# Kernel tuning notes

Hardware: AMD Instinct MI355X
Metric: run time of the kernel (lower is better)

Reference implementation:

```python
import jax, jax.numpy as jnp
import numpy as np

LOWER_T = 6.0
UPPER_T = 50.0


def _conv(x, w, pad_h, pad_w):
    # x: [N,1,H,W] or [N,Cin,H,W]; w: [O,I,kh,kw]; cross-correlation like torch Conv2d
    return jax.lax.conv_general_dilated(
        x, w, window_strides=(1, 1),
        padding=[(pad_h, pad_h), (pad_w, pad_w)],
        dimension_numbers=('NCHW', 'OIHW', 'NCHW'))


def setup_inputs() -> dict:
    key = jax.random.key(0)
    H = W = 4096
    img = jax.random.uniform(key, (1, 3, H, W), dtype=jnp.float32) * 255.0

    # scipy.signal.gaussian(5, std=1.0), unnormalized window
    std = 1.0
    g = np.exp(-0.5 * ((np.arange(5, dtype=np.float32) - 2.0) / std) ** 2).astype(np.float32)
    gauss = jnp.asarray(g)  # [5]

    sobel = jnp.asarray(np.array([[1, 0, -1], [2, 0, -2], [1, 0, -1]], dtype=np.float32))  # [3,3]

    f = np.zeros((8, 1, 3, 3), dtype=np.float32)
    f[:, 0, 1, 1] = 1.0
    offs = [(1, 2), (2, 2), (2, 1), (2, 0), (1, 0), (0, 0), (0, 1), (0, 2)]  # 0,45,...,315 deg
    for k, (r, c) in enumerate(offs):
        f[k, 0, r, c] = -1.0
    dir_w = jnp.asarray(f)  # [8,1,3,3]

    return {"img": img, "gauss": gauss, "sobel": sobel, "dir_w": dir_w}


def reference(img, gauss, sobel, dir_w):
    N, C, H, W = img.shape  # N == 1, C == 3
    x = img.reshape(C, 1, H, W)  # treat channels as batch

    # separable gaussian blur: 1x5 then 5x1, padding 2 (matches torch Conv2d)
    gw_h = gauss.reshape(1, 1, 1, 5)
    gw_v = gauss.reshape(1, 1, 5, 1)
    blurred = _conv(_conv(x, gw_h, 0, 2), gw_v, 2, 0)  # [3,1,H,W]

    sw_h = sobel.reshape(1, 1, 3, 3)
    sw_v = sobel.T.reshape(1, 1, 3, 3)
    gx = _conv(blurred, sw_h, 1, 1)  # [3,1,H,W]
    gy = _conv(blurred, sw_v, 1, 1)

    # per-channel magnitude summed over RGB -> [1,1,H,W]
    grad_mag = jnp.sqrt(gx * gx + gy * gy + 1e-8).sum(axis=0, keepdims=True)[:, 0:1]

    gx_sum = gx.sum(axis=0, keepdims=True)[:, 0:1]
    gy_sum = gy.sum(axis=0, keepdims=True)[:, 0:1]
    ori = jnp.arctan2(gy_sum, gx_sum) * (180.0 / 3.14159) + 180.0
    ori = jnp.round(ori / 45.0) * 45.0

    all_filtered = _conv(grad_mag, dir_w, 1, 1)  # [1,8,H,W]

    idx_pos = jnp.mod(ori / 45.0, 8.0).astype(jnp.int32)          # [1,1,H,W]
    idx_neg = jnp.mod(ori / 45.0 + 4.0, 8.0).astype(jnp.int32)

    cs_pos = jnp.take_along_axis(all_filtered, idx_pos, axis=1)  # [1,1,H,W]
    cs_neg = jnp.take_along_axis(all_filtered, idx_neg, axis=1)

    is_max = jnp.minimum(cs_pos, cs_neg) > 0.0

    thin = jnp.where(is_max, grad_mag, 0.0)
    keep = is_max & (thin >= LOWER_T) & (thin <= UPPER_T)
    thresholded = jnp.where(keep, 1.0, 0.0).astype(jnp.float32)  # [1,1,H,W]
    return thresholded
```

## Files before the change

### kernel.cpp

```cpp
#include <hip/hip_runtime.h>


#define IMG_H 4096
#define IMG_W 4096

constexpr int TW = 32, TH = 32;
constexpr int HBH = 40, HBW = 40;
constexpr int BH  = 36, BW  = 40;
constexpr int MH  = 34, MW  = 36;

__global__ __launch_bounds__(256, 6)
void canny_fused(const float* __restrict__ img,
                 const float* __restrict__ gauss,
                 float* __restrict__ out) {
  __shared__ float s_hb[HBH * HBW];
  __shared__ float s_bl[BH * BW];
  __shared__ float s_bs[BH * BW];
  __shared__ float s_mg[MH * MW];

  const int tid = threadIdx.x;
  const int X0 = blockIdx.x * TW;
  const int Y0 = blockIdx.y * TH;

  const float g0 = gauss[0], g1 = gauss[1], g2 = gauss[2],
              g3 = gauss[3], g4 = gauss[4];

  for (int ch = 0; ch < 3; ++ch) {
    const float* im = img + (size_t)ch * ((size_t)IMG_H * IMG_W);

    for (int j = tid; j < HBH * 10; j += 256) {
      int r = j / 10, g = j - r * 10;
      int c0 = g * 4;
      int gy = Y0 - 4 + r;
      float4 o;
      if ((unsigned)gy < IMG_H) {
        int cb = X0 - 4 + c0;
        const float* row = im + (size_t)gy * IMG_W;
        float a0, a1, a2, a3, a4, a5, a6, a7;
        if (cb >= 0 && cb + 7 < IMG_W) {
          float4 va = *(const float4*)(row + cb);
          float4 vb = *(const float4*)(row + cb + 4);
          a0 = va.x; a1 = va.y; a2 = va.z; a3 = va.w;
          a4 = vb.x; a5 = vb.y; a6 = vb.z; a7 = vb.w;
        } else {
          float t[8];
#pragma unroll
          for (int u = 0; u < 8; ++u) {
            int x = cb + u;
            t[u] = ((unsigned)x < IMG_W) ? row[x] : 0.f;
          }
          a0 = t[0]; a1 = t[1]; a2 = t[2]; a3 = t[3];
          a4 = t[4]; a5 = t[5]; a6 = t[6]; a7 = t[7];
        }
        o.x = g0 * a0 + g1 * a1 + g2 * a2 + g3 * a3 + g4 * a4;
        o.y = g0 * a1 + g1 * a2 + g2 * a3 + g3 * a4 + g4 * a5;
        o.z = g0 * a2 + g1 * a3 + g2 * a4 + g3 * a5 + g4 * a6;
        o.w = g0 * a3 + g1 * a4 + g2 * a5 + g3 * a6 + g4 * a7;
      } else {
        o = make_float4(0.f, 0.f, 0.f, 0.f);
      }
      *(float4*)&s_hb[r * HBW + c0] = o;
    }
    __syncthreads();

    for (int j = tid; j < BH * 10; j += 256) {
      int r = j / 10, g = j - r * 10;
      int c0 = g * 4;
      float4 a0 = *(const float4*)&s_hb[(r    ) * HBW + c0];
      float4 a1 = *(const float4*)&s_hb[(r + 1) * HBW + c0];
      float4 a2 = *(const float4*)&s_hb[(r + 2) * HBW + c0];
      float4 a3 = *(const float4*)&s_hb[(r + 3) * HBW + c0];
      float4 a4 = *(const float4*)&s_hb[(r + 4) * HBW + c0];
      float4 v;
      v.x = g0 * a0.x + g1 * a1.x + g2 * a2.x + g3 * a3.x + g4 * a4.x;
      v.y = g0 * a0.y + g1 * a1.y + g2 * a2.y + g3 * a3.y + g4 * a4.y;
      v.z = g0 * a0.z + g1 * a1.z + g2 * a2.z + g3 * a3.z + g4 * a4.z;
      v.w = g0 * a0.w + g1 * a1.w + g2 * a2.w + g3 * a3.w + g4 * a4.w;
      int gy = Y0 - 2 + r;
      bool rok = (unsigned)gy < IMG_H;
      int gx0 = X0 - 2 + c0;
      v.x = (rok && (unsigned)(gx0    ) < IMG_W) ? v.x : 0.f;
      v.y = (rok && (unsigned)(gx0 + 1) < IMG_W) ? v.y : 0.f;
      v.z = (rok && (unsigned)(gx0 + 2) < IMG_W) ? v.z : 0.f;
      v.w = (rok && (unsigned)(gx0 + 3) < IMG_W) ? v.w : 0.f;
      *(float4*)&s_bl[r * BW + c0] = v;
      float4* ps = (float4*)&s_bs[r * BW + c0];
      if (ch == 0) {
        *ps = v;
      } else {
        float4 s = *ps;
        s.x += v.x; s.y += v.y; s.z += v.z; s.w += v.w;
        *ps = s;
      }
    }
    __syncthreads();

    for (int j = tid; j < MH * 9; j += 256) {
      int r = j / 9, g = j - r * 9;
      int c0 = g * 4;
      float w0[6], w1[6], w2[6];
      {
        float4 p = *(const float4*)&s_bl[(r    ) * BW + c0];
        float2 q = *(const float2*)&s_bl[(r    ) * BW + c0 + 4];
        w0[0]=p.x; w0[1]=p.y; w0[2]=p.z; w0[3]=p.w; w0[4]=q.x; w0[5]=q.y;
      }
      {
        float4 p = *(const float4*)&s_bl[(r + 1) * BW + c0];
        float2 q = *(const float2*)&s_bl[(r + 1) * BW + c0 + 4];
        w1[0]=p.x; w1[1]=p.y; w1[2]=p.z; w1[3]=p.w; w1[4]=q.x; w1[5]=q.y;
      }
      {
        float4 p = *(const float4*)&s_bl[(r + 2) * BW + c0];
        float2 q = *(const float2*)&s_bl[(r + 2) * BW + c0 + 4];
        w2[0]=p.x; w2[1]=p.y; w2[2]=p.z; w2[3]=p.w; w2[4]=q.x; w2[5]=q.y;
      }
      int gy = Y0 - 1 + r;
      bool rok = (unsigned)gy < IMG_H;
      float res[4];
#pragma unroll
      for (int e = 0; e < 4; ++e) {
        float gxv = w0[e] - w0[e + 2] + 2.f * w1[e] - 2.f * w1[e + 2] + w2[e] - w2[e + 2];
        float gyv = w0[e] + 2.f * w0[e + 1] + w0[e + 2] - w2[e] - 2.f * w2[e + 1] - w2[e + 2];
        float m = sqrtf(gxv * gxv + gyv * gyv + 1e-8f);
        int gx = X0 - 1 + c0 + e;
        res[e] = (rok && (unsigned)gx < IMG_W) ? m : 0.f;
      }
      float4* pd = (float4*)&s_mg[r * MW + c0];
      if (ch == 0) {
        *pd = make_float4(res[0], res[1], res[2], res[3]);
      } else {
        float4 s = *pd;
        s.x += res[0]; s.y += res[1]; s.z += res[2]; s.w += res[3];
        *pd = s;
      }
    }
    __syncthreads();
  }

  {
    const int ty  = tid >> 3;
    const int tx0 = (tid & 7) << 2;
    const int row1 = (ty + 1) * MW;

    float4 q0 = *(const float4*)&s_mg[row1 + tx0];
    float4 q1 = *(const float4*)&s_mg[row1 + tx0 + 4];
    float mcs[4];
    mcs[0] = q0.y; mcs[1] = q0.z; mcs[2] = q0.w; mcs[3] = q1.x;

    bool band = false;
#pragma unroll
    for (int e = 0; e < 4; ++e)
      band = band || (mcs[e] >= 6.0f && mcs[e] <= 50.0f);

    float4 resv = make_float4(0.f, 0.f, 0.f, 0.f);
    if (__ballot(band) != 0ULL) {
      float w0[8], w1[8], w2[8];
#pragma unroll
      for (int rr = 0; rr < 3; ++rr) {
        float* w = (rr == 0) ? w0 : (rr == 1) ? w1 : w2;
        float4 p = *(const float4*)&s_bs[(ty + 1 + rr) * BW + tx0];
        float4 q = *(const float4*)&s_bs[(ty + 1 + rr) * BW + tx0 + 4];
        w[0]=p.x; w[1]=p.y; w[2]=p.z; w[3]=p.w; w[4]=q.x; w[5]=q.y; w[6]=q.z; w[7]=q.w;
      }
      const unsigned long long off_tbl = 0xDDDCDBFF23242501ULL;
      float res[4];
#pragma unroll
      for (int e = 0; e < 4; ++e) {
        int tx = tx0 + e;
        float b00 = w0[e + 1], b01 = w0[e + 2], b02 = w0[e + 3];
        float b10 = w1[e + 1],                  b12 = w1[e + 3];
        float b20 = w2[e + 1], b21 = w2[e + 2], b22 = w2[e + 3];
        float gxs = b00 - b02 + 2.f * b10 - 2.f * b12 + b20 - b22;
        float gys = b00 + 2.f * b01 + b02 - b20 - 2.f * b21 - b22;
        float ax = fabsf(gxs), ay = fabsf(gys);
        float f1 = ay - 0.41421356f * ax;
        float f2 = ay - 2.4142137f * ax;
        int off;
        if (fminf(fabsf(f1), fabsf(f2)) < 1e-4f * (ax + ay)) {
          float ori = atan2f(gys, gxs) * 57.295827908797776f + 180.0f;
          int k = (int)rintf(ori / 45.0f);
          int ip = k & 7;
          off = (int)(signed char)(off_tbl >> (ip * 8));
        } else {
          off = (f1 <= 0.f) ? 1
              : (f2 >= 0.f) ? MW
              : (((__float_as_uint(gxs) ^ __float_as_uint(gys)) >> 31) ? (MW - 1)
                                                                       : (MW + 1));
        }
        int ctr = row1 + (tx + 1);
        float mc  = mcs[e];
        float csp = mc - s_mg[ctr + off];
        float csn = mc - s_mg[ctr - off];
        bool is_max = fminf(csp, csn) > 0.0f;
        bool keep = is_max && (mc >= 6.0f) && (mc <= 50.0f);
        res[e] = keep ? 1.0f : 0.0f;
      }
      resv = make_float4(res[0], res[1], res[2], res[3]);
    }
    *(float4*)&out[(size_t)(Y0 + ty) * IMG_W + (X0 + tx0)] = resv;
  }
}

extern "C" void kernel_launch(void* const* d_in, const int* in_sizes, int n_in,
                              void* d_out, int out_size, void* d_ws, size_t ws_size,
                              hipStream_t stream) {
  const float* img   = (const float*)d_in[0];
  const float* gauss = (const float*)d_in[1];
  float* out = (float*)d_out;
  dim3 grid(IMG_W / TW, IMG_H / TH);
  canny_fused<<<grid, 256, 0, stream>>>(img, gauss, out);
}
```

Measured before the change: 345.7 us.

## Prefetch next channel's loads into registers and specialize interior blocks

The per-channel loop is restructured so the global loads for the next channel are issued into registers before the current channel's vertical blur and Sobel stages run, overlapping memory latency with compute. The cross-channel sums for the blur and magnitude are kept in registers and written to shared memory only on the last channel, removing shared read-modify-write traffic. A template specialization drops all boundary checks for interior tiles. In exchange, more registers stay live across stages, which could reduce occupancy under the 6-blocks-per-CU launch bound.

```diff
diff --git a/kernel.cpp b/kernel.cpp
--- a/kernel.cpp
+++ b/kernel.cpp
@@ -9,131 +9,158 @@
 constexpr int BH  = 36, BW  = 40;
 constexpr int MH  = 34, MW  = 36;
 
-__global__ __launch_bounds__(256, 6)
-void canny_fused(const float* __restrict__ img,
-                 const float* __restrict__ gauss,
-                 float* __restrict__ out) {
-  __shared__ float s_hb[HBH * HBW];
-  __shared__ float s_bl[BH * BW];
-  __shared__ float s_bs[BH * BW];
-  __shared__ float s_mg[MH * MW];
-
-  const int tid = threadIdx.x;
-  const int X0 = blockIdx.x * TW;
-  const int Y0 = blockIdx.y * TH;
-
-  const float g0 = gauss[0], g1 = gauss[1], g2 = gauss[2],
-              g3 = gauss[3], g4 = gauss[4];
-
-  for (int ch = 0; ch < 3; ++ch) {
+template<bool INTERIOR>
+__device__ __forceinline__ void pipeline(
+    const float* __restrict__ img,
+    float g0, float g1, float g2, float g3, float g4,
+    int X0, int Y0, int tid,
+    float* __restrict__ s_hb, float* __restrict__ s_bl,
+    float* __restrict__ s_bs, float* __restrict__ s_mg,
+    float* __restrict__ out) {
+
+  const int rA0 = tid / 10, cA0 = (tid - rA0 * 10) * 4;
+  const int jA1 = tid + 256;
+  const int rA1 = jA1 / 10, cA1 = (jA1 - rA1 * 10) * 4;
+  const bool hasA1 = (tid < 144);
+  const bool hasB1 = (tid < 104);
+  const int rC0 = tid / 9,  cC0 = (tid - rC0 * 9) * 4;
+  const int jC1 = tid + 256;
+  const int rC1 = jC1 / 9,  cC1 = (jC1 - rC1 * 9) * 4;
+  const bool hasC1 = (tid < 50);
+
+  float4 pa0, pb0, pa1, pb1;
+  float4 bsA0, bsA1, mgA0, mgA1;
+
+  auto prefA = [&](int ch) {
     const float* im = img + (size_t)ch * ((size_t)IMG_H * IMG_W);
-
-    for (int j = tid; j < HBH * 10; j += 256) {
-      int r = j / 10, g = j - r * 10;
-      int c0 = g * 4;
-      int gy = Y0 - 4 + r;
+    if (INTERIOR) {
+      const float* r0 = im + (size_t)(Y0 - 4 + rA0) * IMG_W + (X0 - 4 + cA0);
+      pa0 = *(const float4*)r0;
+      pb0 = *(const float4*)(r0 + 4);
+      if (hasA1) {
+        const float* r1 = im + (size_t)(Y0 - 4 + rA1) * IMG_W + (X0 - 4 + cA1);
+        pa1 = *(const float4*)r1;
+        pb1 = *(const float4*)(r1 + 4);
+      }
+    } else {
+      auto ld = [&](int r, int c0, float4& va, float4& vb) {
+        va = make_float4(0.f, 0.f, 0.f, 0.f);
+        vb = make_float4(0.f, 0.f, 0.f, 0.f);
+        int gy = Y0 - 4 + r;
+        if ((unsigned)gy < IMG_H) {
+          int cb = X0 - 4 + c0;
+          const float* row = im + (size_t)gy * IMG_W;
+          if (cb >= 0 && cb + 7 < IMG_W) {
+            va = *(const float4*)(row + cb);
+            vb = *(const float4*)(row + cb + 4);
+          } else {
+            float t[8];
+#pragma unroll
+            for (int u = 0; u < 8; ++u) {
+              int x = cb + u;
+              t[u] = ((unsigned)x < IMG_W) ? row[x] : 0.f;
+            }
+            va = make_float4(t[0], t[1], t[2], t[3]);
+            vb = make_float4(t[4], t[5], t[6], t[7]);
+          }
+        }
+      };
+      ld(rA0, cA0, pa0, pb0);
+      if (hasA1) ld(rA1, cA1, pa1, pb1);
+    }
+  };
+
+  auto computeA = [&]() {
+    auto h5 = [&](const float4& a, const float4& b) {
       float4 o;
-      if ((unsigned)gy < IMG_H) {
-        int cb = X0 - 4 + c0;
-        const float* row = im + (size_t)gy * IMG_W;
-        float a0, a1, a2, a3, a4, a5, a6, a7;
-        if (cb >= 0 && cb + 7 < IMG_W) {
-          float4 va = *(const float4*)(row + cb);
-          float4 vb = *(const float4*)(row + cb + 4);
-          a0 = va.x; a1 = va.y; a2 = va.z; a3 = va.w;
-          a4 = vb.x; a5 = vb.y; a6 = vb.z; a7 = vb.w;
-        } else {
-          float t[8];
-#pragma unroll
-          for (int u = 0; u < 8; ++u) {
-            int x = cb + u;
-            t[u] = ((unsigned)x < IMG_W) ? row[x] : 0.f;
-          }
-          a0 = t[0]; a1 = t[1]; a2 = t[2]; a3 = t[3];
-          a4 = t[4]; a5 = t[5]; a6 = t[6]; a7 = t[7];
-        }
-        o.x = g0 * a0 + g1 * a1 + g2 * a2 + g3 * a3 + g4 * a4;
-        o.y = g0 * a1 + g1 * a2 + g2 * a3 + g3 * a4 + g4 * a5;
-        o.z = g0 * a2 + g1 * a3 + g2 * a4 + g3 * a5 + g4 * a6;
-        o.w = g0 * a3 + g1 * a4 + g2 * a5 + g3 * a6 + g4 * a7;
-      } else {
-        o = make_float4(0.f, 0.f, 0.f, 0.f);
-      }
-      *(float4*)&s_hb[r * HBW + c0] = o;
-    }
-    __syncthreads();
-
-    for (int j = tid; j < BH * 10; j += 256) {
-      int r = j / 10, g = j - r * 10;
-      int c0 = g * 4;
-      float4 a0 = *(const float4*)&s_hb[(r    ) * HBW + c0];
-      float4 a1 = *(const float4*)&s_hb[(r + 1) * HBW + c0];
-      float4 a2 = *(const float4*)&s_hb[(r + 2) * HBW + c0];
-      float4 a3 = *(const float4*)&s_hb[(r + 3) * HBW + c0];
-      float4 a4 = *(const float4*)&s_hb[(r + 4) * HBW + c0];
+      o.x = g0 * a.x + g1 * a.y + g2 * a.z + g3 * a.w + g4 * b.x;
+      o.y = g0 * a.y + g1 * a.z + g2 * a.w + g3 * b.x + g4 * b.y;
+      o.z = g0 * a.z + g1 * a.w + g2 * b.x + g3 * b.y + g4 * b.z;
+      o.w = g0 * a.w + g1 * b.x + g2 * b.y + g3 * b.z + g4 * b.w;
+      return o;
+    };
+    *(float4*)&s_hb[rA0 * HBW + cA0] = h5(pa0, pb0);
+    if (hasA1) *(float4*)&s_hb[rA1 * HBW + cA1] = h5(pa1, pb1);
+  };
+
+  auto stageB = [&](int ch) {
+    auto doB = [&](int r, int c0, float4& acc) {
+      const float* p = &s_hb[r * HBW + c0];
+      float4 a0 = *(const float4*)(p);
+      float4 a1 = *(const float4*)(p + HBW);
+      float4 a2 = *(const float4*)(p + 2 * HBW);
+      float4 a3 = *(const float4*)(p + 3 * HBW);
+      float4 a4 = *(const float4*)(p + 4 * HBW);
       float4 v;
       v.x = g0 * a0.x + g1 * a1.x + g2 * a2.x + g3 * a3.x + g4 * a4.x;
       v.y = g0 * a0.y + g1 * a1.y + g2 * a2.y + g3 * a3.y + g4 * a4.y;
       v.z = g0 * a0.z + g1 * a1.z + g2 * a2.z + g3 * a3.z + g4 * a4.z;
       v.w = g0 * a0.w + g1 * a1.w + g2 * a2.w + g3 * a3.w + g4 * a4.w;
-      int gy = Y0 - 2 + r;
-      bool rok = (unsigned)gy < IMG_H;
-      int gx0 = X0 - 2 + c0;
-      v.x = (rok && (unsigned)(gx0    ) < IMG_W) ? v.x : 0.f;
-      v.y = (rok && (unsigned)(gx0 + 1) < IMG_W) ? v.y : 0.f;
-      v.z = (rok && (unsigned)(gx0 + 2) < IMG_W) ? v.z : 0.f;
-      v.w = (rok && (unsigned)(gx0 + 3) < IMG_W) ? v.w : 0.f;
+      if (!INTERIOR) {
+        int gy = Y0 - 2 + r;
+        bool rok = (unsigned)gy < IMG_H;
+        int gx0 = X0 - 2 + c0;
+        v.x = (rok && (unsigned)(gx0    ) < IMG_W) ? v.x : 0.f;
+        v.y = (rok && (unsigned)(gx0 + 1) < IMG_W) ? v.y : 0.f;
+        v.z = (rok && (unsigned)(gx0 + 2) < IMG_W) ? v.z : 0.f;
+        v.w = (rok && (unsigned)(gx0 + 3) < IMG_W) ? v.w : 0.f;
+      }
       *(float4*)&s_bl[r * BW + c0] = v;
-      float4* ps = (float4*)&s_bs[r * BW + c0];
       if (ch == 0) {
-        *ps = v;
+        acc = v;
       } else {
-        float4 s = *ps;
-        s.x += v.x; s.y += v.y; s.z += v.z; s.w += v.w;
-        *ps = s;
-      }
-    }
-    __syncthreads();
-
-    for (int j = tid; j < MH * 9; j += 256) {
-      int r = j / 9, g = j - r * 9;
-      int c0 = g * 4;
+        acc.x += v.x; acc.y += v.y; acc.z += v.z; acc.w += v.w;
+      }
+      if (ch == 2) *(float4*)&s_bs[r * BW + c0] = acc;
+    };
+    doB(rA0, cA0, bsA0);
+    if (hasB1) doB(rA1, cA1, bsA1);
+  };
+
+  auto stageC = [&](int ch) {
+    auto doC = [&](int r, int c0, float4& acc) {
       float w0[6], w1[6], w2[6];
-      {
-        float4 p = *(const float4*)&s_bl[(r    ) * BW + c0];
-        float2 q = *(const float2*)&s_bl[(r    ) * BW + c0 + 4];
-        w0[0]=p.x; w0[1]=p.y; w0[2]=p.z; w0[3]=p.w; w0[4]=q.x; w0[5]=q.y;
-      }
-      {
-        float4 p = *(const float4*)&s_bl[(r + 1) * BW + c0];
-        float2 q = *(const float2*)&s_bl[(r + 1) * BW + c0 + 4];
-        w1[0]=p.x; w1[1]=p.y; w1[2]=p.z; w1[3]=p.w; w1[4]=q.x; w1[5]=q.y;
-      }
-      {
-        float4 p = *(const float4*)&s_bl[(r + 2) * BW + c0];
-        float2 q = *(const float2*)&s_bl[(r + 2) * BW + c0 + 4];
-        w2[0]=p.x; w2[1]=p.y; w2[2]=p.z; w2[3]=p.w; w2[4]=q.x; w2[5]=q.y;
-      }
-      int gy = Y0 - 1 + r;
-      bool rok = (unsigned)gy < IMG_H;
+      const float* p = &s_bl[r * BW + c0];
+      { float4 a = *(const float4*)p;            float2 b = *(const float2*)(p + 4);
+        w0[0]=a.x; w0[1]=a.y; w0[2]=a.z; w0[3]=a.w; w0[4]=b.x; w0[5]=b.y; }
+      { float4 a = *(const float4*)(p + BW);     float2 b = *(const float2*)(p + BW + 4);
+        w1[0]=a.x; w1[1]=a.y; w1[2]=a.z; w1[3]=a.w; w1[4]=b.x; w1[5]=b.y; }
+      { float4 a = *(const float4*)(p + 2 * BW); float2 b = *(const float2*)(p + 2 * BW + 4);
+        w2[0]=a.x; w2[1]=a.y; w2[2]=a.z; w2[3]=a.w; w2[4]=b.x; w2[5]=b.y; }
       float res[4];
 #pragma unroll
       for (int e = 0; e < 4; ++e) {
         float gxv = w0[e] - w0[e + 2] + 2.f * w1[e] - 2.f * w1[e + 2] + w2[e] - w2[e + 2];
         float gyv = w0[e] + 2.f * w0[e + 1] + w0[e + 2] - w2[e] - 2.f * w2[e + 1] - w2[e + 2];
         float m = sqrtf(gxv * gxv + gyv * gyv + 1e-8f);
-        int gx = X0 - 1 + c0 + e;
-        res[e] = (rok && (unsigned)gx < IMG_W) ? m : 0.f;
-      }
-      float4* pd = (float4*)&s_mg[r * MW + c0];
+        if (!INTERIOR) {
+          int gy = Y0 - 1 + r;
+          int gx = X0 - 1 + c0 + e;
+          m = ((unsigned)gy < IMG_H && (unsigned)gx < IMG_W) ? m : 0.f;
+        }
+        res[e] = m;
+      }
       if (ch == 0) {
-        *pd = make_float4(res[0], res[1], res[2], res[3]);
+        acc = make_float4(res[0], res[1], res[2], res[3]);
       } else {
-        float4 s = *pd;
-        s.x += res[0]; s.y += res[1]; s.z += res[2]; s.w += res[3];
-        *pd = s;
-      }
-    }
+        acc.x += res[0]; acc.y += res[1]; acc.z += res[2]; acc.w += res[3];
+      }
+      if (ch == 2) *(float4*)&s_mg[r * MW + c0] = acc;
+    };
+    doC(rC0, cC0, mgA0);
+    if (hasC1) doC(rC1, cC1, mgA1);
+  };
+
+  prefA(0);
+  computeA();
+  __syncthreads();
+#pragma unroll
+  for (int ch = 0; ch < 3; ++ch) {
+    if (ch < 2) prefA(ch + 1);
+    stageB(ch);
+    __syncthreads();
+    stageC(ch);
+    if (ch < 2) computeA();
     __syncthreads();
   }
 
@@ -201,6 +228,29 @@
   }
 }
 
+__global__ __launch_bounds__(256, 6)
+void canny_fused(const float* __restrict__ img,
+                 const float* __restrict__ gauss,
+                 float* __restrict__ out) {
+  __shared__ float s_hb[HBH * HBW];
+  __shared__ float s_bl[BH * BW];
+  __shared__ float s_bs[BH * BW];
+  __shared__ float s_mg[MH * MW];
+
+  const int tid = threadIdx.x;
+  const int X0 = blockIdx.x * TW;
+  const int Y0 = blockIdx.y * TH;
+  const float g0 = gauss[0], g1 = gauss[1], g2 = gauss[2],
+              g3 = gauss[3], g4 = gauss[4];
+
+  const bool interior = (blockIdx.x >= 1) && (blockIdx.x <= 126) &&
+                        (blockIdx.y >= 1) && (blockIdx.y <= 126);
+  if (interior)
+    pipeline<true >(img, g0, g1, g2, g3, g4, X0, Y0, tid, s_hb, s_bl, s_bs, s_mg, out);
+  else
+    pipeline<false>(img, g0, g1, g2, g3, g4, X0, Y0, tid, s_hb, s_bl, s_bs, s_mg, out);
+}
+
 extern "C" void kernel_launch(void* const* d_in, const int* in_sizes, int n_in,
                               void* d_out, int out_size, void* d_ws, size_t ws_size,
                               hipStream_t stream) {
```

New measurement: 517.9 us. 1.5x slower.
